# Kernel optimization log

Measured on AMD Instinct MI355X. Metric: run time of the kernel, lower is better.

Reference implementation:

```python
import jax, jax.numpy as jnp
import numpy as np

N, T, NC, D = 256, 20, 1, 32
NF, Q, VSTEPS, HDYN = 16, 32, 10, 256
HDIM = NF * 64           # n_filt * 4**3
DT = 0.1
BETA = 1.0
LOG2PI = float(np.log(2.0 * np.pi))


def conv2d(x, w, b):
    # k=4, s=2, p=1 : halves spatial dims. x: [B,Cin,H,W], w: [Cout,Cin,4,4]
    y = jax.lax.conv_general_dilated(x, w, (2, 2), [(1, 1), (1, 1)],
                                     dimension_numbers=('NCHW', 'OIHW', 'NCHW'))
    return y + b[None, :, None, None]


def deconv2d(x, w, b):
    # stride-2 transposed conv, doubles spatial dims. w: [Cout,Cin,4,4]
    y = jax.lax.conv_transpose(x, w, (2, 2), 'SAME',
                               dimension_numbers=('NCHW', 'OIHW', 'NCHW'))
    return y + b[None, :, None, None]


def encode(x, C1, c1, C2, c2, C3, c3, Wm, bm, Wl, bl):
    h = jax.nn.relu(conv2d(x, C1, c1))
    h = jax.nn.relu(conv2d(h, C2, c2))
    h = jax.nn.relu(conv2d(h, C3, c3))   # [B, 4*NF, 4, 4]
    h = h.reshape(h.shape[0], -1)        # [B, HDIM]
    return h @ Wm + bm, h @ Wl + bl


def setup_inputs() -> dict:
    key = jax.random.key(0)
    ks = jax.random.split(key, 40)
    r = lambda i, shape, s=0.05: s * jax.random.normal(ks[i], shape, jnp.float32)
    inp = {
        'X': jax.random.uniform(ks[0], (N, T, NC, D, D), jnp.float32),
        'eps_s0': jax.random.normal(ks[1], (N, Q), jnp.float32),
        'eps_v0': jax.random.normal(ks[2], (N, Q), jnp.float32),
        # enc_s (input = 1 frame)
        'Cs1': r(3, (NF, NC, 4, 4)), 'cs1': jnp.zeros((NF,)),
        'Cs2': r(4, (2 * NF, NF, 4, 4)), 'cs2': jnp.zeros((2 * NF,)),
        'Cs3': r(5, (4 * NF, 2 * NF, 4, 4)), 'cs3': jnp.zeros((4 * NF,)),
        'Wsm': r(6, (HDIM, Q)), 'bsm': jnp.zeros((Q,)),
        'Wsl': r(7, (HDIM, Q), 0.01), 'bsl': -1.0 * jnp.ones((Q,)),
        # enc_v (input = v_steps frames stacked as channels)
        'Cv1': r(8, (NF, VSTEPS * NC, 4, 4)), 'cv1': jnp.zeros((NF,)),
        'Cv2': r(9, (2 * NF, NF, 4, 4)), 'cv2': jnp.zeros((2 * NF,)),
        'Cv3': r(10, (4 * NF, 2 * NF, 4, 4)), 'cv3': jnp.zeros((4 * NF,)),
        'Wvm': r(11, (HDIM, Q)), 'bvm': jnp.zeros((Q,)),
        'Wvl': r(12, (HDIM, Q), 0.01), 'bvl': -1.0 * jnp.ones((Q,)),
        # dynamics f : R^{2q} -> R^q (tanh MLP)
        'W1': r(13, (2 * Q, HDYN), 0.1), 'b1': jnp.zeros((HDYN,)),
        'W2': r(14, (HDYN, Q), 0.1), 'b2': jnp.zeros((Q,)),
        # fc3 + decoder
        'Wf': r(15, (Q, HDIM)), 'bf': jnp.zeros((HDIM,)),
        'D1': r(16, (2 * NF, 4 * NF, 4, 4)), 'd1': jnp.zeros((2 * NF,)),
        'D2': r(17, (NF, 2 * NF, 4, 4)), 'd2': jnp.zeros((NF,)),
        'D3': r(18, (NC, NF, 4, 4)), 'd3': jnp.zeros((NC,)),
        'Ndata': 10000,
    }
    return inp


def reference(X, eps_s0, eps_v0,
              Cs1, cs1, Cs2, cs2, Cs3, cs3, Wsm, bsm, Wsl, bsl,
              Cv1, cv1, Cv2, cv2, Cv3, cv3, Wvm, bvm, Wvl, bvl,
              W1, b1, W2, b2, Wf, bf, D1, d1, D2, d2, D3, d3, Ndata):
    Nb, Tt = X.shape[0], X.shape[1]
    # ---- encode z0 = [v0, s0]
    s0_mu, s0_lv = encode(X[:, 0], Cs1, cs1, Cs2, cs2, Cs3, cs3, Wsm, bsm, Wsl, bsl)
    xv = X[:, :VSTEPS].reshape(Nb, VSTEPS * NC, D, D)
    v0_mu, v0_lv = encode(xv, Cv1, cv1, Cv2, cv2, Cv3, cv3, Wvm, bvm, Wvl, bvl)
    s0 = s0_mu + eps_s0 * jnp.exp(s0_lv)
    v0 = v0_mu + eps_v0 * jnp.exp(v0_lv)
    # standard-normal density of the base noise (q dims each)
    logp0 = (-0.5 * jnp.sum(eps_s0 ** 2, -1) - 0.5 * Q * LOG2PI) + \
            (-0.5 * jnp.sum(eps_v0 ** 2, -1) - 0.5 * Q * LOG2PI)
    z0 = jnp.concatenate([v0, s0], axis=1)               # [N,2q]
    qz0_m = jnp.concatenate([v0_mu, s0_mu], axis=1)
    qz0_logv = jnp.concatenate([v0_lv, s0_lv], axis=1)

    # ---- augmented ODE rhs: dz = [f(z), v], dlogp = -tr(df/dv)
    # exact trace for the tanh MLP: J = W2^T diag(1-h^2) W1^T, so
    # tr_{i<q} J = (1-h^2) @ c with c_k = sum_{i<q} W1[i,k] * W2[k,i]
    c = jnp.sum(W1[:Q] * W2.T, axis=0)                   # [HDYN]

    def rhs(vs):
        h = jnp.tanh(vs @ W1 + b1)                       # [N,HDYN]
        dv = h @ W2 + b2                                 # [N,q]
        dvs = jnp.concatenate([dv, vs[:, :Q]], axis=1)   # [N,2q]
        tr = (1.0 - h * h) @ c                           # [N]
        return dvs, -tr

    def rk4_step(carry, _):
        z, lp = carry
        k1z, k1l = rhs(z)
        k2z, k2l = rhs(z + 0.5 * DT * k1z)
        k3z, k3l = rhs(z + 0.5 * DT * k2z)
        k4z, k4l = rhs(z + DT * k3z)
        z2 = z + (DT / 6.0) * (k1z + 2 * k2z + 2 * k3z + k4z)
        lp2 = lp + (DT / 6.0) * (k1l + 2 * k2l + 2 * k3l + k4l)
        return (z2, lp2), (z2, lp2)

    (_, _), (zs, lps) = jax.lax.scan(rk4_step, (z0, logp0), None, length=Tt - 1)
    zt = jnp.concatenate([z0[None], zs], axis=0)         # [T,N,2q]
    logp = jnp.concatenate([logp0[None], lps], axis=0)   # [T,N]
    ztL = jnp.transpose(zt, (1, 0, 2))[None]             # [1,N,T,2q] (L=1)
    logpL = logp.T[None]                                 # [1,N,T]

    # ---- decode positions s_t
    s = ztL[..., Q:].reshape(-1, Q) @ Wf + bf            # [N*T, HDIM]
    h = s.reshape(-1, 4 * NF, 4, 4)
    h = jax.nn.relu(deconv2d(h, D1, d1))                 # [N*T,2NF,8,8]
    h = jax.nn.relu(deconv2d(h, D2, d2))                 # [N*T,NF,16,16]
    Xrec = jax.nn.sigmoid(deconv2d(h, D3, d3))           # [N*T,NC,32,32]
    Xrec = Xrec.reshape(1, Nb, Tt, NC, D, D)

    # ---- ELBO
    log_pzt = -0.5 * jnp.sum(ztL ** 2, -1) - Q * LOG2PI  # N(0,I) over 2q dims
    kl_z = (logpL - log_pzt).sum(2).mean(0)              # [N]
    lhood_L = jnp.log(0.001 + Xrec) * X[None] + jnp.log(1.001 - Xrec) * (1.0 - X[None])
    lhood = lhood_L.sum((2, 3, 4, 5)).mean(0)            # [N]
    kl_w = 0.5 * (jnp.sum(W1 ** 2) + jnp.sum(W2 ** 2))
    Nd = jnp.float32(Ndata)
    lh = Nd * lhood.mean()
    klz = Nd * kl_z.mean()
    elbo = lh - klz - BETA * kl_w
    return Xrec, qz0_m, qz0_logv, ztL, elbo, lh, klz, BETA * kl_w


if __name__ == '__main__':
    outs = reference(**setup_inputs())
    print(outs[0].shape, float(outs[4]))
```

## Files before the change

kernel.cpp:

```cpp
#include <hip/hip_runtime.h>
#include <math.h>

#define N_S 256
#define T_S 20
#define D_S 32
#define NF_S 16
#define Q_S 32
#define HDYN_S 256
#define HDIM_S 1024
#define VSTEPS_S 10
#define DT_S 0.1f
#define LOG2PI_F 1.8378770664093453f

#define OUT_XREC 0
#define OUT_QM   5242880
#define OUT_QLV  5259264
#define OUT_ZT   5275648
#define OUT_SCAL 5603328

#define OS_A1S   0
#define OS_A2S   1048576

#define WS_A1V   0
#define WS_WT2   32768
#define WS_WT3   40960
#define WS_A2V   1048576
#define WS_M1    1048576
#define WS_C1    1114112
#define WS_S0MU  1572864
#define WS_S0LV  1581056
#define WS_V0MU  1589248
#define WS_V0LV  1597440
#define WS_LHOOD 1610752
#define WS_KLZ   1611008
#define WS_TC    1611520
#define TC_S1 (WS_TC + 0)
#define TC_V1 (WS_TC + 256)
#define TC_S2 (WS_TC + 2816)
#define TC_V2 (WS_TC + 11008)
#define TC_S3 (WS_TC + 19200)
#define TC_V3 (WS_TC + 51968)

__device__ inline void enc_tr(const float* __restrict__ src, float* __restrict__ dst,
                              int e, int CI, int CO) {
    int co = e % CO; int r = e / CO; int tap = r & 15; int ci = r >> 4;
    dst[e] = src[(co * CI + ci) * 16 + tap];
}
__device__ inline void dec_tr(const float* __restrict__ src, float* __restrict__ dst,
                              int e, int CI, int CO) {
    int co = e % CO; int r = e / CO; int ci = r % CI; int tap = r / CI;
    dst[e] = src[(co * CI + ci) * 16 + tap];
}

__global__ __launch_bounds__(256) void prep_enc(
    const float* __restrict__ Cs1, const float* __restrict__ Cv1,
    const float* __restrict__ Cs2, const float* __restrict__ Cv2,
    const float* __restrict__ Cs3, const float* __restrict__ Cv3,
    float* __restrict__ ws)
{
    int blk = blockIdx.x, t = threadIdx.x;
    if (blk < 331) {
        int idx = blk * 256 + t;
        if (blk == 0) ws[WS_LHOOD + t] = 0.f;
        if (idx < 256)        enc_tr(Cs1, ws + TC_S1, idx,          1, 16);
        else if (idx < 2816)  enc_tr(Cv1, ws + TC_V1, idx - 256,   10, 16);
        else if (idx < 11008) enc_tr(Cs2, ws + TC_S2, idx - 2816,  16, 32);
        else if (idx < 19200) enc_tr(Cv2, ws + TC_V2, idx - 11008, 16, 32);
        else if (idx < 51968) enc_tr(Cs3, ws + TC_S3, idx - 19200, 32, 64);
        else if (idx < 84736) enc_tr(Cv3, ws + TC_V3, idx - 51968, 32, 64);
    } else {
        int zi = (blk - 331) * 256 + t;
        ws[WS_S0MU + zi] = 0.f;
    }
}

__global__ __launch_bounds__(256) void conv1_both(
    const float* __restrict__ x,
    const float* __restrict__ wts, const float* __restrict__ bs, float* __restrict__ outs,
    const float* __restrict__ wtv, const float* __restrict__ bv, float* __restrict__ outv)
{
    __shared__ float xin[10 * 630];
    int sel = blockIdx.z;
    int cin = sel ? 10 : 1;
    const float* wt = sel ? wtv : wts;
    const float* bias = sel ? bv : bs;
    float* out = sel ? outv : outs;

    int b = blockIdx.x, yh = blockIdx.y, t = threadIdx.x;
    for (int e = t; e < cin * 576; e += 256) {
        int ci = e / 576;
        int r = (e >> 5) - ci * 18;
        int cx = e & 31;
        int gy = yh * 16 - 1 + r;
        float v = (gy >= 0 && gy < 32) ? x[(size_t)b * 20480 + ci * 1024 + gy * 32 + cx] : 0.f;
        xin[ci * 630 + r * 35 + cx + 1] = v;
    }
    for (int e = t; e < cin * 18; e += 256) {
        int ci = e / 18, r = e - ci * 18;
        xin[ci * 630 + r * 35 + 0] = 0.f;
        xin[ci * 630 + r * 35 + 33] = 0.f;
    }
    __syncthreads();

    int ocq = __builtin_amdgcn_readfirstlane(t >> 7);
    int p = t & 127;
    int oyl = p >> 4, ox = p & 15;
    const float* wg = wt + ocq * 8;
    float acc[8];
    #pragma unroll
    for (int j = 0; j < 8; j++) acc[j] = bias[ocq * 8 + j];
    for (int ci = 0; ci < cin; ci++) {
        const float* xc = xin + ci * 630;
        const float* wc = wg + ci * 256;
        #pragma unroll
        for (int ky = 0; ky < 4; ky++) {
            const float* xr = xc + (2 * oyl + ky) * 35;
            #pragma unroll
            for (int kx = 0; kx < 4; kx++) {
                float v = xr[2 * ox + kx];
                const float4* w4 = (const float4*)(wc + (ky * 4 + kx) * 16);
                float4 wa = w4[0], wb2 = w4[1];
                acc[0] = fmaf(v, wa.x, acc[0]);
                acc[1] = fmaf(v, wa.y, acc[1]);
                acc[2] = fmaf(v, wa.z, acc[2]);
                acc[3] = fmaf(v, wa.w, acc[3]);
                acc[4] = fmaf(v, wb2.x, acc[4]);
                acc[5] = fmaf(v, wb2.y, acc[5]);
                acc[6] = fmaf(v, wb2.z, acc[6]);
                acc[7] = fmaf(v, wb2.w, acc[7]);
            }
        }
    }
    int oy = yh * 8 + oyl;
    size_t ob = (size_t)b * 4096 + (size_t)(ocq * 8) * 256 + oy * 16 + ox;
    #pragma unroll
    for (int j = 0; j < 8; j++) out[ob + (size_t)j * 256] = fmaxf(acc[j], 0.f);
}

__global__ __launch_bounds__(256) void conv2_both(
    const float* __restrict__ a1s, const float* __restrict__ wts, const float* __restrict__ bsb,
    float* __restrict__ outs,
    const float* __restrict__ a1v, const float* __restrict__ wtv, const float* __restrict__ bvb,
    float* __restrict__ outv)
{
    __shared__ float xin[16 * 272];
    int sel = blockIdx.z;
    const float* a1 = sel ? a1v : a1s;
    const float* wt = sel ? wtv : wts;
    const float* bias = sel ? bvb : bsb;
    float* out = sel ? outv : outs;

    int b = blockIdx.x, h = blockIdx.y, t = threadIdx.x;
    for (int e = t; e < 4096; e += 256) {
        int ci = e >> 8, r = e & 255, iy = r >> 4, ix = r & 15;
        xin[ci * 272 + iy * 17 + ix] = a1[(size_t)b * 4096 + e];
    }
    __syncthreads();

    int ocq = __builtin_amdgcn_readfirstlane(t >> 6);
    int p = t & 63;
    int pa = p >> 3, pb = p & 7;
    int hbase = h * 16 + ocq * 4;
    float acc[4];
    #pragma unroll
    for (int j = 0; j < 4; j++) acc[j] = bias[hbase + j];
    for (int ci = 0; ci < 16; ci++) {
        const float* xc = xin + ci * 272;
        const float* wc = wt + ci * 512 + hbase;
        #pragma unroll
        for (int ky = 0; ky < 4; ky++) {
            int iy = 2 * pa - 1 + ky;
            if ((unsigned)iy >= 16u) continue;
            const float* xr = xc + iy * 17;
            #pragma unroll
            for (int kx = 0; kx < 4; kx++) {
                int ix = 2 * pb - 1 + kx;
                if ((unsigned)ix >= 16u) continue;
                float v = xr[ix];
                float4 wv = *(const float4*)(wc + (ky * 4 + kx) * 32);
                acc[0] = fmaf(v, wv.x, acc[0]);
                acc[1] = fmaf(v, wv.y, acc[1]);
                acc[2] = fmaf(v, wv.z, acc[2]);
                acc[3] = fmaf(v, wv.w, acc[3]);
            }
        }
    }
    size_t ob = (size_t)b * 2048 + (size_t)(hbase) * 64 + pa * 8 + pb;
    #pragma unroll
    for (int j = 0; j < 4; j++) out[ob + (size_t)j * 64] = fmaxf(acc[j], 0.f);
}

__global__ __launch_bounds__(256) void conv3fc_both(
    const float* __restrict__ a2s, const float* __restrict__ wts,
    const float* __restrict__ bsb,
    const float* __restrict__ Wsm, const float* __restrict__ Wsl,
    float* __restrict__ mus, float* __restrict__ lvs,
    const float* __restrict__ a2v, const float* __restrict__ wtv,
    const float* __restrict__ bvb,
    const float* __restrict__ Wvm, const float* __restrict__ Wvl,
    float* __restrict__ muv, float* __restrict__ lvv)
{
    __shared__ float xin[32 * 72];
    __shared__ float wl[16384];
    __shared__ float bl[32];
    __shared__ float hbuf[512];
    __shared__ float pr[256];
    int sel = blockIdx.z;
    const float* a2 = sel ? a2v : a2s;
    const float* wt = sel ? wtv : wts;
    const float* bias = sel ? bvb : bsb;

    int b = blockIdx.x, h = blockIdx.y, t = threadIdx.x;
    for (int e = t; e < 2048; e += 256) {
        int ci = e >> 6, r = e & 63, iy = r >> 3, ix = r & 7;
        xin[ci * 72 + iy * 9 + ix] = a2[(size_t)b * 2048 + e];
    }
    for (int e4 = t; e4 < 4096; e4 += 256) {
        int grp = e4 >> 3, c4 = e4 & 7;
        ((float4*)wl)[e4] = ((const float4*)(wt + grp * 64 + h * 32))[c4];
    }
    if (t < 32) bl[t] = bias[h * 32 + t];
    __syncthreads();

    int ocq = t >> 4, p = t & 15;
    int pa = p >> 2, pb = p & 3;
    float a0 = bl[ocq * 2], a1 = bl[ocq * 2 + 1];
    for (int ci = 0; ci < 32; ci++) {
        const float* xc = xin + ci * 72;
        const float* wc = wl + ci * 512 + ocq * 2;
        #pragma unroll
        for (int ky = 0; ky < 4; ky++) {
            int iy = 2 * pa - 1 + ky;
            if ((unsigned)iy >= 8u) continue;
            const float* xr = xc + iy * 9;
            #pragma unroll
            for (int kx = 0; kx < 4; kx++) {
                int ix = 2 * pb - 1 + kx;
                if ((unsigned)ix >= 8u) continue;
                float v = xr[ix];
                float2 wv = *(const float2*)(wc + (ky * 4 + kx) * 32);
                a0 = fmaf(v, wv.x, a0);
                a1 = fmaf(v, wv.y, a1);
            }
        }
    }
    int lp_ = ocq * 32 + p;
    hbuf[lp_]      = fmaxf(a0, 0.f);
    hbuf[lp_ + 16] = fmaxf(a1, 0.f);
    __syncthreads();

    {
        int q = t & 63, c = t >> 6, qq = q & 31;
        const float* Wb = (q < 32) ? (sel ? Wvm : Wsm) : (sel ? Wvl : Wsl);
        const float* wp = Wb + (size_t)(h * 512 + c * 128) * 32 + qq;
        const float* hp = hbuf + c * 128;
        float s = 0.f;
        #pragma unroll 4
        for (int k = 0; k < 128; k++) s = fmaf(hp[k], wp[(size_t)k * 32], s);
        pr[c * 64 + q] = s;
    }
    __syncthreads();
    if (t < 64) {
        float s = (pr[t] + pr[64 + t]) + (pr[128 + t] + pr[192 + t]);
        float* dst = (t < 32) ? (sel ? muv : mus) : (sel ? lvv : lvs);
        atomicAdd(&dst[b * 32 + (t & 31)], s);
    }
}

__global__ __launch_bounds__(256) void ode_kernel(
    const float* __restrict__ W1, const float* __restrict__ b1,
    const float* __restrict__ W2, const float* __restrict__ b2,
    const float* __restrict__ s0mu_a, const float* __restrict__ s0lv_a,
    const float* __restrict__ v0mu_a, const float* __restrict__ v0lv_a,
    const float* __restrict__ bsm, const float* __restrict__ bsl,
    const float* __restrict__ bvm, const float* __restrict__ bvl,
    const float* __restrict__ eps_s, const float* __restrict__ eps_v,
    const float* __restrict__ Wf, const float* __restrict__ bf,
    const float* __restrict__ D1, const float* __restrict__ d1,
    const float* __restrict__ D2, const float* __restrict__ D3,
    float* __restrict__ ws,
    float* __restrict__ qm, float* __restrict__ qlv,
    float* __restrict__ ztL, float* __restrict__ klz)
{
    __shared__ float W2s[HDYN_S * Q_S];
    __shared__ float zeval[64];
    __shared__ float hsh[HDYN_S];
    __shared__ float dvred[HDYN_S];
    __shared__ float red4[4];
    int n = blockIdx.x;
    int t = threadIdx.x;

    if (n >= 256) {
        float* shA = W2s;
        float* shB = W2s + 4096;
        int m = n - 256;
        if (m < 64) {
            int j = m >> 3, q4 = m & 7;
            for (int e = t; e < 4096; e += 256) {
                int qq = e >> 10, k = e & 1023;
                shA[e] = Wf[(size_t)(q4 * 4 + qq) * 1024 + k];
            }
            for (int e = t; e < 4096; e += 256) {
                int ocg = e >> 10, r = e & 1023;
                shB[e] = D1[(size_t)(ocg * 8 + j) * 1024 + r];
            }
            __syncthreads();
            int p = t & 63, ocg = t >> 6;
            int y = p >> 3, x = p & 7;
            float acc[4] = {0.f, 0.f, 0.f, 0.f};
            #pragma unroll
            for (int sy = 0; sy < 2; sy++) {
                int ky = (y & 1) + 2 * sy;
                int iy = ((y + ky) >> 1) - 1;
                if ((unsigned)iy >= 4u) continue;
                #pragma unroll
                for (int sx = 0; sx < 2; sx++) {
                    int kx = (x & 1) + 2 * sx;
                    int ix = ((x + kx) >> 1) - 1;
                    if ((unsigned)ix >= 4u) continue;
                    const float* dl = shB + ocg * 1024 + ky * 4 + kx;
                    const float* wl = shA + iy * 4 + ix;
                    for (int ci = 0; ci < 64; ci++) {
                        float wv = dl[ci * 16];
                        int kb = ci * 16;
                        acc[0] = fmaf(wl[kb],        wv, acc[0]);
                        acc[1] = fmaf(wl[1024 + kb], wv, acc[1]);
                        acc[2] = fmaf(wl[2048 + kb], wv, acc[2]);
                        acc[3] = fmaf(wl[3072 + kb], wv, acc[3]);
                    }
                }
            }
            ((float4*)(ws + WS_M1))[m * 256 + t] = make_float4(acc[0], acc[1], acc[2], acc[3]);
        } else if (m < 80) {
            int bb = m - 64;
            for (int e = t; e < 1024; e += 256) shA[e] = bf[e];
            for (int e = t; e < 2048; e += 256) shB[e] = D1[(size_t)bb * 2048 + e];
            __syncthreads();
            int oidx = t >> 1, half = t & 1;
            int ocr = oidx >> 6, p = oidx & 63;
            int y = p >> 3, x = p & 7;
            float acc = 0.f;
            #pragma unroll
            for (int sy = 0; sy < 2; sy++) {
                int ky = (y & 1) + 2 * sy;
                int iy = ((y + ky) >> 1) - 1;
                if ((unsigned)iy >= 4u) continue;
                #pragma unroll
                for (int sx = 0; sx < 2; sx++) {
                    int kx = (x & 1) + 2 * sx;
                    int ix = ((x + kx) >> 1) - 1;
                    if ((unsigned)ix >= 4u) continue;
                    const float* dl = shB + ocr * 1024 + half * 512 + ky * 4 + kx;
                    const float* wl = shA + half * 512 + iy * 4 + ix;
                    for (int cc = 0; cc < 32; cc++)
                        acc = fmaf(wl[cc * 16], dl[cc * 16], acc);
                }
            }
            acc += __shfl_down(acc, 1, 64);
            if (half == 0) {
                int oc = bb * 2 + ocr;
                ws[WS_C1 + (oc & 7) * 256 + (oc >> 3) * 64 + p] = acc + d1[oc];
            }
        } else {
            int idx = (m - 80) * 256 + t;
            if (idx < 8192)      dec_tr(D2, ws + WS_WT2, idx,        32, 16);
            else if (idx < 8448) dec_tr(D3, ws + WS_WT3, idx - 8192, 16, 1);
        }
        return;
    }

    for (int i = t; i < HDYN_S * Q_S; i += 256) W2s[i] = W2[i];
    float w1r[64];
    #pragma unroll
    for (int j = 0; j < 64; j++) w1r[j] = W1[j * HDYN_S + t];
    float b1r = b1[t];
    __syncthreads();
    float ck = 0.f;
    #pragma unroll
    for (int i = 0; i < Q_S; i++) ck = fmaf(w1r[i], W2s[t * Q_S + i], ck);

    size_t zoff = (size_t)n * T_S * 64;
    float zj = 0.f, ksumj = 0.f, zevalj = 0.f, lp = 0.f, lsum = 0.f, klacc = 0.f;

    if (t < 64) {
        int q = t & 31;
        float mu, lvv2, ep;
        if (t < 32) { mu = v0mu_a[n*32+q] + bvm[q]; lvv2 = v0lv_a[n*32+q] + bvl[q]; ep = eps_v[n*32+q]; }
        else        { mu = s0mu_a[n*32+q] + bsm[q]; lvv2 = s0lv_a[n*32+q] + bsl[q]; ep = eps_s[n*32+q]; }
        float zv = fmaf(ep, expf(lvv2), mu);
        qm[n*64 + t]  = mu;
        qlv[n*64 + t] = lvv2;
        zj = zv; zevalj = zv; zeval[t] = zv;
        ztL[zoff + t] = zv;
        float e2 = ep * ep;
        float z2 = zv * zv;
        #pragma unroll
        for (int off = 32; off; off >>= 1) {
            e2 += __shfl_down(e2, off, 64);
            z2 += __shfl_down(z2, off, 64);
        }
        if (t == 0) {
            lp = -0.5f * e2 - Q_S * LOG2PI_F;
            klacc = lp - (-0.5f * z2 - Q_S * LOG2PI_F);
        }
    }

    const float wc[4] = {1.f, 2.f, 2.f, 1.f};
    const float ac[3] = {0.5f * DT_S, 0.5f * DT_S, DT_S};
    const float4* ze4 = (const float4*)zeval;

    for (int step = 1; step < T_S; step++) {
        for (int e = 0; e < 4; e++) {
            __syncthreads();
            float p0 = 0.f, p1 = 0.f, p2 = 0.f, p3 = 0.f;
            #pragma unroll
            for (int j4 = 0; j4 < 4; j4++) {
                float4 za = ze4[j4], zb = ze4[4 + j4], zc = ze4[8 + j4], zd = ze4[12 + j4];
                p0 = fmaf(za.x, w1r[j4*4+0], p0);
                p0 = fmaf(za.y, w1r[j4*4+1], p0);
                p0 = fmaf(za.z, w1r[j4*4+2], p0);
                p0 = fmaf(za.w, w1r[j4*4+3], p0);
                p1 = fmaf(zb.x, w1r[16+j4*4+0], p1);
                p1 = fmaf(zb.y, w1r[16+j4*4+1], p1);
                p1 = fmaf(zb.z, w1r[16+j4*4+2], p1);
                p1 = fmaf(zb.w, w1r[16+j4*4+3], p1);
                p2 = fmaf(zc.x, w1r[32+j4*4+0], p2);
                p2 = fmaf(zc.y, w1r[32+j4*4+1], p2);
                p2 = fmaf(zc.z, w1r[32+j4*4+2], p2);
                p2 = fmaf(zc.w, w1r[32+j4*4+3], p2);
                p3 = fmaf(zd.x, w1r[48+j4*4+0], p3);
                p3 = fmaf(zd.y, w1r[48+j4*4+1], p3);
                p3 = fmaf(zd.z, w1r[48+j4*4+2], p3);
                p3 = fmaf(zd.w, w1r[48+j4*4+3], p3);
            }
            float pre = b1r + ((p0 + p1) + (p2 + p3));
            float hk = tanhf(pre);
            hsh[t] = hk;
            float gk = (1.f - hk * hk) * ck;
            #pragma unroll
            for (int off = 32; off; off >>= 1) gk += __shfl_down(gk, off, 64);
            if ((t & 63) == 0) red4[t >> 6] = gk;
            __syncthreads();
            {
                int i = t & 31, p = t >> 5;
                const float4* h4 = (const float4*)(hsh + p * 32);
                float a0 = 0.f, a1 = 0.f;
                #pragma unroll
                for (int kk4 = 0; kk4 < 4; kk4++) {
                    float4 ha = h4[kk4];
                    float4 hb2 = h4[4 + kk4];
                    int kb = p * 32 + kk4 * 4;
                    a0 = fmaf(ha.x, W2s[(kb+0)*Q_S + i], a0);
                    a0 = fmaf(ha.y, W2s[(kb+1)*Q_S + i], a0);
                    a0 = fmaf(ha.z, W2s[(kb+2)*Q_S + i], a0);
                    a0 = fmaf(ha.w, W2s[(kb+3)*Q_S + i], a0);
                    int kc = kb + 16;
                    a1 = fmaf(hb2.x, W2s[(kc+0)*Q_S + i], a1);
                    a1 = fmaf(hb2.y, W2s[(kc+1)*Q_S + i], a1);
                    a1 = fmaf(hb2.z, W2s[(kc+2)*Q_S + i], a1);
                    a1 = fmaf(hb2.w, W2s[(kc+3)*Q_S + i], a1);
                }
                dvred[t] = a0 + a1;
            }
            __syncthreads();
            if (t < 64) {
                float tr = red4[0] + red4[1] + red4[2] + red4[3];
                float zv_shfl = __shfl(zevalj, (t >= 32) ? (t - 32) : t, 64);
                float kzv;
                if (t < 32) {
                    float dvi = b2[t];
                    #pragma unroll
                    for (int p = 0; p < 8; p++) dvi += dvred[p * 32 + t];
                    kzv = dvi;
                } else kzv = zv_shfl;
                if (e == 0) ksumj = kzv; else ksumj = fmaf(wc[e], kzv, ksumj);
                if (t == 0) { float kl = -tr; lsum = (e == 0) ? kl : fmaf(wc[e], kl, lsum); }
                if (e < 3) {
                    zevalj = fmaf(ac[e], kzv, zj);
                    zeval[t] = zevalj;
                } else {
                    zj = fmaf(DT_S / 6.f, ksumj, zj);
                    zevalj = zj; zeval[t] = zj;
                    ztL[zoff + step * 64 + t] = zj;
                    if (t == 0) lp = fmaf(DT_S / 6.f, lsum, lp);
                    float z2 = zj * zj;
                    #pragma unroll
                    for (int off = 32; off; off >>= 1) z2 += __shfl_down(z2, off, 64);
                    if (t == 0) klacc += lp - (-0.5f * z2 - Q_S * LOG2PI_F);
                }
            }
        }
    }
    if (t == 0) klz[n] = klacc;
}

__global__ __launch_bounds__(256) void decoder5(
    const float* __restrict__ ztL, const float* __restrict__ M1L, const float* __restrict__ c1L,
    const float* __restrict__ wt2, const float* __restrict__ d2,
    const float* __restrict__ wt3, const float* __restrict__ d3,
    const float* __restrict__ X, float* __restrict__ Xrec, float* __restrict__ lhood)
{
    __shared__ float zs[32];
    __shared__ float regA[3600];
    __shared__ float regB[4160];
    __shared__ float sh4[4];
    float* h2f = regB;
    float* h1f = regA;
    float* xst = regA;
    const int bidx = blockIdx.x;
    const int t = threadIdx.x;
    const int wu = __builtin_amdgcn_readfirstlane(t >> 6);
    const int l = t & 63;
    const int py = wu >> 1, px = wu & 1;

    if (t < 32) zs[t] = ztL[(size_t)bidx * 64 + 32 + t];
    {
        float4 z4 = make_float4(0.f, 0.f, 0.f, 0.f);
        for (int e = t; e < 900; e += 256) ((float4*)regA)[e] = z4;
    }
    __syncthreads();

    {
        float acc[8];
        #pragma unroll
        for (int j = 0; j < 8; j++) acc[j] = c1L[j * 256 + t];
        const float4* M14 = (const float4*)M1L;
        #pragma unroll
        for (int q4 = 0; q4 < 8; q4++) {
            float4 z4 = *(const float4*)(zs + q4 * 4);
            #pragma unroll
            for (int j = 0; j < 8; j++) {
                float4 m = M14[(j * 8 + q4) * 256 + t];
                acc[j] = fmaf(z4.x, m.x, fmaf(z4.y, m.y, fmaf(z4.z, m.z, fmaf(z4.w, m.w, acc[j]))));
            }
        }
        int p = t & 63, ocg = t >> 6;
        int y = p >> 3, x = p & 7;
        float* hp = h1f + (y + 1) * 360 + (x + 1) * 36 + ocg * 8;
        float4 r0, r1;
        r0.x = fmaxf(acc[0], 0.f); r0.y = fmaxf(acc[1], 0.f);
        r0.z = fmaxf(acc[2], 0.f); r0.w = fmaxf(acc[3], 0.f);
        r1.x = fmaxf(acc[4], 0.f); r1.y = fmaxf(acc[5], 0.f);
        r1.z = fmaxf(acc[6], 0.f); r1.w = fmaxf(acc[7], 0.f);
        *(float4*)(hp)     = r0;
        *(float4*)(hp + 4) = r1;
    }
    __syncthreads();

    {
        int a = l >> 3, b = l & 7;
        float acc[16];
        #pragma unroll
        for (int j = 0; j < 16; j++) acc[j] = d2[j];
        #pragma unroll
        for (int sy = 0; sy < 2; sy++) {
            int ky = py + 2 * sy;
            int iyf = a + py + sy - 1;
            #pragma unroll
            for (int sx = 0; sx < 2; sx++) {
                int kx = px + 2 * sx;
                int ixf = b + px + sx - 1;
                const float4* ip4 = (const float4*)(h1f + (iyf + 1) * 360 + (ixf + 1) * 36);
                const float* wb = wt2 + (ky * 4 + kx) * 512;
                #pragma unroll 2
                for (int cc = 0; cc < 8; cc++) {
                    float4 v = ip4[cc];
                    float vv[4] = {v.x, v.y, v.z, v.w};
                    #pragma unroll
                    for (int r = 0; r < 4; r++) {
                        const float4* wq = (const float4*)(wb + (cc * 4 + r) * 16);
                        float4 w0 = wq[0], w1 = wq[1], w2 = wq[2], w3 = wq[3];
                        float vr = vv[r];
                        acc[0]  = fmaf(vr, w0.x, acc[0]);
                        acc[1]  = fmaf(vr, w0.y, acc[1]);
                        acc[2]  = fmaf(vr, w0.z, acc[2]);
                        acc[3]  = fmaf(vr, w0.w, acc[3]);
                        acc[4]  = fmaf(vr, w1.x, acc[4]);
                        acc[5]  = fmaf(vr, w1.y, acc[5]);
                        acc[6]  = fmaf(vr, w1.z, acc[6]);
                        acc[7]  = fmaf(vr, w1.w, acc[7]);
                        acc[8]  = fmaf(vr, w2.x, acc[8]);
                        acc[9]  = fmaf(vr, w2.y, acc[9]);
                        acc[10] = fmaf(vr, w2.z, acc[10]);
                        acc[11] = fmaf(vr, w2.w, acc[11]);
                        acc[12] = fmaf(vr, w3.x, acc[12]);
                        acc[13] = fmaf(vr, w3.y, acc[13]);
                        acc[14] = fmaf(vr, w3.z, acc[14]);
                        acc[15] = fmaf(vr, w3.w, acc[15]);
                    }
                }
            }
        }
        float* hq = h2f + (2 * a + py) * 260 + (2 * b + px) * 16;
        #pragma unroll
        for (int j = 0; j < 4; j++) {
            float4 r;
            r.x = fmaxf(acc[j*4+0], 0.f);
            r.y = fmaxf(acc[j*4+1], 0.f);
            r.z = fmaxf(acc[j*4+2], 0.f);
            r.w = fmaxf(acc[j*4+3], 0.f);
            *(float4*)(hq + j * 4) = r;
        }
    }
    __syncthreads();

    {
        int oy2 = l >> 2, b3 = l & 3;
        float acc[4];
        float d30 = d3[0];
        #pragma unroll
        for (int k = 0; k < 4; k++) acc[k] = d30;
        #pragma unroll
        for (int sy = 0; sy < 2; sy++) {
            int ky = py + 2 * sy;
            int iy = oy2 + py + sy - 1;
            if ((unsigned)iy >= 16u) continue;
            #pragma unroll
            for (int sx = 0; sx < 2; sx++) {
                int kx = px + 2 * sx;
                int cx = px + sx - 1;
                const float* wvp = wt3 + (ky * 4 + kx) * 16;
                #pragma unroll
                for (int k = 0; k < 4; k++) {
                    int ix = b3 + 4 * k + cx;
                    if ((unsigned)ix >= 16u) continue;
                    const float4* in4 = (const float4*)(h2f + iy * 260 + ix * 16);
                    #pragma unroll
                    for (int cc = 0; cc < 4; cc++) {
                        float4 v = in4[cc];
                        float4 wq = ((const float4*)wvp)[cc];
                        acc[k] = fmaf(v.x, wq.x, acc[k]);
                        acc[k] = fmaf(v.y, wq.y, acc[k]);
                        acc[k] = fmaf(v.z, wq.z, acc[k]);
                        acc[k] = fmaf(v.w, wq.w, acc[k]);
                    }
                }
            }
        }
        int oy = 2 * oy2 + py;
        #pragma unroll
        for (int k = 0; k < 4; k++) {
            int ox = 2 * (b3 + 4 * k) + px;
            xst[oy * 36 + ox] = 1.f / (1.f + expf(-acc[k]));
        }
    }
    __syncthreads();

    {
        int row = t >> 3, col = (t & 7) * 4;
        float4 xr4 = *(const float4*)(xst + row * 36 + col);
        *(float4*)(Xrec + (size_t)bidx * 1024 + t * 4) = xr4;
        float4 xi4 = *(const float4*)(X + (size_t)bidx * 1024 + t * 4);
        float ll = 0.f;
        ll += logf(0.001f + xr4.x) * xi4.x + logf(1.001f - xr4.x) * (1.f - xi4.x);
        ll += logf(0.001f + xr4.y) * xi4.y + logf(1.001f - xr4.y) * (1.f - xi4.y);
        ll += logf(0.001f + xr4.z) * xi4.z + logf(1.001f - xr4.z) * (1.f - xi4.z);
        ll += logf(0.001f + xr4.w) * xi4.w + logf(1.001f - xr4.w) * (1.f - xi4.w);
        #pragma unroll
        for (int off = 32; off; off >>= 1) ll += __shfl_down(ll, off, 64);
        if ((t & 63) == 0) sh4[t >> 6] = ll;
    }
    __syncthreads();
    if (t == 0) atomicAdd(&lhood[bidx / T_S], sh4[0] + sh4[1] + sh4[2] + sh4[3]);
}

__global__ __launch_bounds__(256) void final2(
    const float* __restrict__ lhood, const float* __restrict__ klz,
    const float* __restrict__ W1, const float* __restrict__ W2,
    const int* __restrict__ Ndata, float* __restrict__ outs)
{
    __shared__ float shA[4], shB[4], shC[4];
    int t = threadIdx.x;
    float a = lhood[t];
    float b = klz[t];
    float c = 0.f;
    for (int i = t; i < 64 * HDYN_S; i += 256) c = fmaf(W1[i], W1[i], c);
    for (int i = t; i < HDYN_S * Q_S; i += 256) c = fmaf(W2[i], W2[i], c);
    #pragma unroll
    for (int off = 32; off; off >>= 1) {
        a += __shfl_down(a, off, 64);
        b += __shfl_down(b, off, 64);
        c += __shfl_down(c, off, 64);
    }
    if ((t & 63) == 0) { shA[t >> 6] = a; shB[t >> 6] = b; shC[t >> 6] = c; }
    __syncthreads();
    if (t == 0) {
        float Nd = (float)Ndata[0];
        float lh = Nd * ((shA[0] + shA[1] + shA[2] + shA[3]) / 256.f);
        float kz = Nd * ((shB[0] + shB[1] + shB[2] + shB[3]) / 256.f);
        float bkw = 0.5f * (shC[0] + shC[1] + shC[2] + shC[3]);
        outs[0] = lh - kz - bkw;
        outs[1] = lh;
        outs[2] = kz;
        outs[3] = bkw;
    }
}

extern "C" void kernel_launch(void* const* d_in, const int* in_sizes, int n_in,
                              void* d_out, int out_size, void* d_ws, size_t ws_size,
                              hipStream_t stream) {
    const float* X      = (const float*)d_in[0];
    const float* eps_s0 = (const float*)d_in[1];
    const float* eps_v0 = (const float*)d_in[2];
    const float* Cs1 = (const float*)d_in[3],  *cs1 = (const float*)d_in[4];
    const float* Cs2 = (const float*)d_in[5],  *cs2 = (const float*)d_in[6];
    const float* Cs3 = (const float*)d_in[7],  *cs3 = (const float*)d_in[8];
    const float* Wsm = (const float*)d_in[9],  *bsm = (const float*)d_in[10];
    const float* Wsl = (const float*)d_in[11], *bsl = (const float*)d_in[12];
    const float* Cv1 = (const float*)d_in[13], *cv1 = (const float*)d_in[14];
    const float* Cv2 = (const float*)d_in[15], *cv2 = (const float*)d_in[16];
    const float* Cv3 = (const float*)d_in[17], *cv3 = (const float*)d_in[18];
    const float* Wvm = (const float*)d_in[19], *bvm = (const float*)d_in[20];
    const float* Wvl = (const float*)d_in[21], *bvl = (const float*)d_in[22];
    const float* W1  = (const float*)d_in[23], *b1  = (const float*)d_in[24];
    const float* W2  = (const float*)d_in[25], *b2  = (const float*)d_in[26];
    const float* Wf  = (const float*)d_in[27], *bf  = (const float*)d_in[28];
    const float* D1  = (const float*)d_in[29], *d1  = (const float*)d_in[30];
    const float* D2  = (const float*)d_in[31], *d2  = (const float*)d_in[32];
    const float* D3  = (const float*)d_in[33], *d3  = (const float*)d_in[34];
    const int*   Ndata = (const int*)d_in[35];

    float* out = (float*)d_out;
    float* ws  = (float*)d_ws;

    float* a1s = out + OS_A1S;
    float* a2s = out + OS_A2S;

    prep_enc<<<459, 256, 0, stream>>>(Cs1, Cv1, Cs2, Cv2, Cs3, Cv3, ws);

    conv1_both<<<dim3(256, 2, 2), 256, 0, stream>>>(X,
        ws + TC_S1, cs1, a1s,
        ws + TC_V1, cv1, ws + WS_A1V);
    conv2_both<<<dim3(256, 2, 2), 256, 0, stream>>>(
        a1s, ws + TC_S2, cs2, a2s,
        ws + WS_A1V, ws + TC_V2, cv2, ws + WS_A2V);
    conv3fc_both<<<dim3(256, 2, 2), 256, 0, stream>>>(
        a2s, ws + TC_S3, cs3, Wsm, Wsl, ws + WS_S0MU, ws + WS_S0LV,
        ws + WS_A2V, ws + TC_V3, cv3, Wvm, Wvl, ws + WS_V0MU, ws + WS_V0LV);

    ode_kernel<<<369, 256, 0, stream>>>(W1, b1, W2, b2,
        ws + WS_S0MU, ws + WS_S0LV, ws + WS_V0MU, ws + WS_V0LV,
        bsm, bsl, bvm, bvl, eps_s0, eps_v0,
        Wf, bf, D1, d1, D2, D3, ws,
        out + OUT_QM, out + OUT_QLV, out + OUT_ZT, ws + WS_KLZ);

    decoder5<<<5120, 256, 0, stream>>>(out + OUT_ZT, ws + WS_M1, ws + WS_C1,
                                       ws + WS_WT2, d2, ws + WS_WT3, d3,
                                       X, out + OUT_XREC, ws + WS_LHOOD);

    final2<<<1, 256, 0, stream>>>(ws + WS_LHOOD, ws + WS_KLZ, W1, W2, Ndata,
                                  out + OUT_SCAL);
}
```

Before: 488.6 us.

## Template conv1 on channel count, unroll conv loops, transpose ODE W2, trim decoder init

conv1 becomes a template on its input-channel count so the channel loop fully unrolls. conv2 and conv3 get unroll pragmas on their channel loops. The ODE kernel stores W2 transposed with a padded stride so each thread reads contiguous float2 weights instead of strided scalar loads. The decoder now zeroes only the halo of its padded shared buffer and reads z directly from global memory, which removes one barrier. The changes are independent micro-optimizations and may raise register pressure.

After: 490.8 us. About the same (+0.4%).

```diff
diff --git a/kernel.cpp b/kernel.cpp
--- a/kernel.cpp
+++ b/kernel.cpp
@@ -74,20 +74,13 @@
     }
 }
 
-__global__ __launch_bounds__(256) void conv1_both(
-    const float* __restrict__ x,
-    const float* __restrict__ wts, const float* __restrict__ bs, float* __restrict__ outs,
-    const float* __restrict__ wtv, const float* __restrict__ bv, float* __restrict__ outv)
+template<int CIN>
+__device__ __forceinline__ void conv1_core(
+    const float* __restrict__ x, const float* __restrict__ wt,
+    const float* __restrict__ bias, float* __restrict__ out,
+    float* xin, int b, int yh, int t)
 {
-    __shared__ float xin[10 * 630];
-    int sel = blockIdx.z;
-    int cin = sel ? 10 : 1;
-    const float* wt = sel ? wtv : wts;
-    const float* bias = sel ? bv : bs;
-    float* out = sel ? outv : outs;
-
-    int b = blockIdx.x, yh = blockIdx.y, t = threadIdx.x;
-    for (int e = t; e < cin * 576; e += 256) {
+    for (int e = t; e < CIN * 576; e += 256) {
         int ci = e / 576;
         int r = (e >> 5) - ci * 18;
         int cx = e & 31;
@@ -95,7 +88,7 @@
         float v = (gy >= 0 && gy < 32) ? x[(size_t)b * 20480 + ci * 1024 + gy * 32 + cx] : 0.f;
         xin[ci * 630 + r * 35 + cx + 1] = v;
     }
-    for (int e = t; e < cin * 18; e += 256) {
+    for (int e = t; e < CIN * 18; e += 256) {
         int ci = e / 18, r = e - ci * 18;
         xin[ci * 630 + r * 35 + 0] = 0.f;
         xin[ci * 630 + r * 35 + 33] = 0.f;
@@ -109,7 +102,8 @@
     float acc[8];
     #pragma unroll
     for (int j = 0; j < 8; j++) acc[j] = bias[ocq * 8 + j];
-    for (int ci = 0; ci < cin; ci++) {
+    #pragma unroll
+    for (int ci = 0; ci < CIN; ci++) {
         const float* xc = xin + ci * 630;
         const float* wc = wg + ci * 256;
         #pragma unroll
@@ -137,6 +131,17 @@
     for (int j = 0; j < 8; j++) out[ob + (size_t)j * 256] = fmaxf(acc[j], 0.f);
 }
 
+__global__ __launch_bounds__(256) void conv1_both(
+    const float* __restrict__ x,
+    const float* __restrict__ wts, const float* __restrict__ bs, float* __restrict__ outs,
+    const float* __restrict__ wtv, const float* __restrict__ bv, float* __restrict__ outv)
+{
+    __shared__ float xin[10 * 630];
+    int b = blockIdx.x, yh = blockIdx.y, t = threadIdx.x;
+    if (blockIdx.z == 0) conv1_core<1>(x, wts, bs, outs, xin, b, yh, t);
+    else                 conv1_core<10>(x, wtv, bv, outv, xin, b, yh, t);
+}
+
 __global__ __launch_bounds__(256) void conv2_both(
     const float* __restrict__ a1s, const float* __restrict__ wts, const float* __restrict__ bsb,
     float* __restrict__ outs,
@@ -164,6 +169,7 @@
     float acc[4];
     #pragma unroll
     for (int j = 0; j < 4; j++) acc[j] = bias[hbase + j];
+    #pragma unroll
     for (int ci = 0; ci < 16; ci++) {
         const float* xc = xin + ci * 272;
         const float* wc = wt + ci * 512 + hbase;
@@ -225,6 +231,7 @@
     int ocq = t >> 4, p = t & 15;
     int pa = p >> 2, pb = p & 3;
     float a0 = bl[ocq * 2], a1 = bl[ocq * 2 + 1];
+    #pragma unroll 4
     for (int ci = 0; ci < 32; ci++) {
         const float* xc = xin + ci * 72;
         const float* wc = wl + ci * 512 + ocq * 2;
@@ -282,7 +289,7 @@
     float* __restrict__ qm, float* __restrict__ qlv,
     float* __restrict__ ztL, float* __restrict__ klz)
 {
-    __shared__ float W2s[HDYN_S * Q_S];
+    __shared__ float W2T[32 * 258];
     __shared__ float zeval[64];
     __shared__ float hsh[HDYN_S];
     __shared__ float dvred[HDYN_S];
@@ -291,8 +298,8 @@
     int t = threadIdx.x;
 
     if (n >= 256) {
-        float* shA = W2s;
-        float* shB = W2s + 4096;
+        float* shA = W2T;
+        float* shB = W2T + 4096;
         int m = n - 256;
         if (m < 64) {
             int j = m >> 3, q4 = m & 7;
@@ -369,7 +376,10 @@
         return;
     }
 
-    for (int i = t; i < HDYN_S * Q_S; i += 256) W2s[i] = W2[i];
+    for (int i = t; i < HDYN_S * Q_S; i += 256) {
+        int k = i >> 5, c = i & 31;
+        W2T[c * 258 + k] = W2[i];
+    }
     float w1r[64];
     #pragma unroll
     for (int j = 0; j < 64; j++) w1r[j] = W1[j * HDYN_S + t];
@@ -377,7 +387,7 @@
     __syncthreads();
     float ck = 0.f;
     #pragma unroll
-    for (int i = 0; i < Q_S; i++) ck = fmaf(w1r[i], W2s[t * Q_S + i], ck);
+    for (int i = 0; i < Q_S; i++) ck = fmaf(w1r[i], W2T[i * 258 + t], ck);
 
     size_t zoff = (size_t)n * T_S * 64;
     float zj = 0.f, ksumj = 0.f, zevalj = 0.f, lp = 0.f, lsum = 0.f, klacc = 0.f;
@@ -443,22 +453,25 @@
             __syncthreads();
             {
                 int i = t & 31, p = t >> 5;
+                const float* wrow = W2T + i * 258 + p * 32;
                 const float4* h4 = (const float4*)(hsh + p * 32);
                 float a0 = 0.f, a1 = 0.f;
                 #pragma unroll
                 for (int kk4 = 0; kk4 < 4; kk4++) {
-                    float4 ha = h4[kk4];
+                    float4 ha  = h4[kk4];
                     float4 hb2 = h4[4 + kk4];
-                    int kb = p * 32 + kk4 * 4;
-                    a0 = fmaf(ha.x, W2s[(kb+0)*Q_S + i], a0);
-                    a0 = fmaf(ha.y, W2s[(kb+1)*Q_S + i], a0);
-                    a0 = fmaf(ha.z, W2s[(kb+2)*Q_S + i], a0);
-                    a0 = fmaf(ha.w, W2s[(kb+3)*Q_S + i], a0);
-                    int kc = kb + 16;
-                    a1 = fmaf(hb2.x, W2s[(kc+0)*Q_S + i], a1);
-                    a1 = fmaf(hb2.y, W2s[(kc+1)*Q_S + i], a1);
-                    a1 = fmaf(hb2.z, W2s[(kc+2)*Q_S + i], a1);
-                    a1 = fmaf(hb2.w, W2s[(kc+3)*Q_S + i], a1);
+                    float2 w0 = *(const float2*)(wrow + kk4 * 4);
+                    float2 w1 = *(const float2*)(wrow + kk4 * 4 + 2);
+                    float2 w2 = *(const float2*)(wrow + 16 + kk4 * 4);
+                    float2 w3 = *(const float2*)(wrow + 16 + kk4 * 4 + 2);
+                    a0 = fmaf(ha.x,  w0.x, a0);
+                    a0 = fmaf(ha.y,  w0.y, a0);
+                    a0 = fmaf(ha.z,  w1.x, a0);
+                    a0 = fmaf(ha.w,  w1.y, a0);
+                    a1 = fmaf(hb2.x, w2.x, a1);
+                    a1 = fmaf(hb2.y, w2.y, a1);
+                    a1 = fmaf(hb2.z, w3.x, a1);
+                    a1 = fmaf(hb2.w, w3.y, a1);
                 }
                 dvred[t] = a0 + a1;
             }
@@ -500,7 +513,6 @@
     const float* __restrict__ wt3, const float* __restrict__ d3,
     const float* __restrict__ X, float* __restrict__ Xrec, float* __restrict__ lhood)
 {
-    __shared__ float zs[32];
     __shared__ float regA[3600];
     __shared__ float regB[4160];
     __shared__ float sh4[4];
@@ -513,21 +525,34 @@
     const int l = t & 63;
     const int py = wu >> 1, px = wu & 1;
 
-    if (t < 32) zs[t] = ztL[(size_t)bidx * 64 + 32 + t];
     {
         float4 z4 = make_float4(0.f, 0.f, 0.f, 0.f);
-        for (int e = t; e < 900; e += 256) ((float4*)regA)[e] = z4;
-    }
-    __syncthreads();
+        for (int e = t; e < 324; e += 256) {
+            int f4i;
+            if (e < 180) {
+                int r = (e < 90) ? 0 : 9;
+                int c = (e < 90) ? e : e - 90;
+                f4i = r * 90 + c;
+            } else {
+                int e2 = e - 180;
+                int row = 1 + (e2 / 18);
+                int wch = e2 % 18;
+                int c = (wch < 9) ? wch : 81 + (wch - 9);
+                f4i = row * 90 + c;
+            }
+            ((float4*)regA)[f4i] = z4;
+        }
+    }
 
     {
+        const float* zp = ztL + (size_t)bidx * 64 + 32;
         float acc[8];
         #pragma unroll
         for (int j = 0; j < 8; j++) acc[j] = c1L[j * 256 + t];
         const float4* M14 = (const float4*)M1L;
         #pragma unroll
         for (int q4 = 0; q4 < 8; q4++) {
-            float4 z4 = *(const float4*)(zs + q4 * 4);
+            float4 z4 = *(const float4*)(zp + q4 * 4);
             #pragma unroll
             for (int j = 0; j < 8; j++) {
                 float4 m = M14[(j * 8 + q4) * 256 + t];
```
